# Optimization experiments

Hardware: AMD Instinct MI355X
Metric: run time of the kernel (lower is better)

Reference implementation:

```python
import jax, jax.numpy as jnp
import numpy as np
from jax import lax

K = 16  # knn_k


def _mlp(x, W1, b1, W2, b2):
    h = jax.nn.gelu(x @ W1 + b1, approximate=False)  # torch nn.GELU default = exact
    return h @ W2 + b2


def setup_inputs() -> dict:
    key = jax.random.key(0)
    ks = jax.random.split(key, 10)
    B, N, F, H = 8, 4096, 64, 128

    def xav(k, shape):
        fan_in = shape[0]
        return (jax.random.normal(k, shape, jnp.float32) / np.sqrt(fan_in)).astype(jnp.float32)

    return {
        "coords": jax.random.normal(ks[0], (B, N, 3), jnp.float32),
        "features": jax.random.normal(ks[1], (B, N, F), jnp.float32),
        "inv_W1": xav(ks[2], (6, H)), "inv_b1": jnp.zeros((H,), jnp.float32),
        "inv_W2": xav(ks[3], (H, H)), "inv_b2": jnp.zeros((H,), jnp.float32),
        "feat_W1": xav(ks[4], (F, H)), "feat_b1": jnp.zeros((H,), jnp.float32),
        "feat_W2": xav(ks[5], (H, H)), "feat_b2": jnp.zeros((H,), jnp.float32),
        "sh_W1": xav(ks[6], (2 * H, H)), "sh_b1": jnp.zeros((H,), jnp.float32),
        "sh_W2": xav(ks[7], (H, H)), "sh_b2": jnp.zeros((H,), jnp.float32),
        "g0_W": xav(ks[8], (H, 1)), "g0_b": jnp.zeros((1,), jnp.float32),
    }


def _local_geometry(coords):
    # coords: [B,N,3]
    B, N, _ = coords.shape
    k = min(K, N - 1)
    # squared pairwise distances (monotone in euclidean dist -> same kNN indices)
    sq = jnp.sum(coords * coords, axis=-1)                    # [B,N]
    dist2 = sq[:, :, None] + sq[:, None, :] - 2.0 * jnp.einsum("bnd,bmd->bnm", coords, coords)
    dist2 = lax.stop_gradient(dist2)
    eye = jnp.eye(N, dtype=bool)
    dist2 = jnp.where(eye[None], jnp.inf, dist2)
    _, idx = lax.top_k(-dist2, k)                             # smallest-k -> [B,N,k]
    neighbors = jax.vmap(lambda c, i: c[i])(coords, idx)      # [B,N,k,3]
    relative = neighbors - coords[:, :, None, :]              # [B,N,k,3]
    cov = jnp.einsum("bnki,bnkj->bnij", relative, relative) / float(k)  # [B,N,3,3]
    evals, evecs = jnp.linalg.eigh(cov)                       # ascending
    normals = evecs[..., 0]                                   # smallest-eigval eigenvector, [B,N,3]
    center = coords.mean(axis=1, keepdims=True)
    outward = coords - center
    orient = jnp.sign(jnp.sum(normals * outward, axis=-1, keepdims=True))
    orient = jnp.where(orient == 0, 1.0, orient)
    normals = normals * orient
    normals = normals / jnp.maximum(jnp.linalg.norm(normals, axis=-1, keepdims=True), 1e-6)
    radius = jnp.linalg.norm(relative, axis=-1).mean(axis=-1, keepdims=True)   # [B,N,1]
    centered_radius = jnp.linalg.norm(outward, axis=-1, keepdims=True)
    eig_sum = jnp.maximum(evals.sum(axis=-1, keepdims=True), 1e-6)
    dominance = evals[..., 2:3] / eig_sum
    invariants = jnp.concatenate([evals, radius, centered_radius, dominance], axis=-1)  # [B,N,6]
    return normals, invariants


def reference(coords, features, inv_W1, inv_b1, inv_W2, inv_b2,
              feat_W1, feat_b1, feat_W2, feat_b2,
              sh_W1, sh_b1, sh_W2, sh_b2, g0_W, g0_b):
    normals, invariants = _local_geometry(coords)
    inv_h = _mlp(invariants, inv_W1, inv_b1, inv_W2, inv_b2)
    feat_h = _mlp(features, feat_W1, feat_b1, feat_W2, feat_b2)
    hidden = _mlp(jnp.concatenate([inv_h, feat_h], axis=-1), sh_W1, sh_b1, sh_W2, sh_b2)
    scalar = hidden @ g0_W + g0_b                                   # grade 0, [B,N,1]
    plane = jnp.stack([normals[..., 0], normals[..., 1], -normals[..., 2],
                       -jnp.sum(coords * normals, axis=-1)], axis=-1)  # grade 1, [B,N,4]
    biv = jnp.concatenate([normals, jnp.zeros_like(normals)], axis=-1)  # grade 2, [B,N,6]
    point = jnp.concatenate([coords, jnp.ones(coords.shape[:-1] + (1,), coords.dtype)], axis=-1)  # grade 3 OPNS point
    zero4 = jnp.zeros(coords.shape[:-1] + (1,), coords.dtype)            # grade 4
    return jnp.concatenate([scalar, plane, biv, point, zero4], axis=-1)  # [B,N,16]
```

## Files before the change

kernel.cpp:

```cpp
#include <hip/hip_runtime.h>
#include <hip/hip_bf16.h>

#define BB 8
#define NN 4096
#define FF 64
#define HH 128
#define KNN 16

typedef __attribute__((ext_vector_type(8))) short bf16x8;
typedef __attribute__((ext_vector_type(4))) float f32x4;

#define OFF_iW2 0
#define OFF_fW1 16384
#define OFF_fW2 24576
#define OFF_sW1 40960
#define OFF_sW2 73728
#define HI_SZ   90112

__device__ __forceinline__ float sq3(float x, float y, float z) {
    return fmaf(z, z, fmaf(y, y, __fmul_rn(x, x)));
}
__device__ __forceinline__ float dist2f(float px, float py, float pz, float psq, float4 cc) {
    float t = fmaf(pz, cc.z, fmaf(py, cc.y, __fmul_rn(px, cc.x)));
    return __fsub_rn(__fadd_rn(psq, cc.w), __fmul_rn(2.0f, t));
}

__device__ __forceinline__ short f2bf(float x) {
    unsigned u = __float_as_uint(x);
    u += 0x7fffu + ((u >> 16) & 1u);
    return (short)(u >> 16);
}
__device__ __forceinline__ float bf2f(short s) {
    return __uint_as_float(((unsigned)(unsigned short)s) << 16);
}

extern "C" __global__ __launch_bounds__(256)
void k_prep(const float* __restrict__ coords, float4* __restrict__ coords4, float* __restrict__ center) {
    const int b = blockIdx.x, tid = threadIdx.x;
    __shared__ float rx[256], ry[256], rz[256];
    float sx = 0.f, sy = 0.f, sz = 0.f;
    for (int n = tid; n < NN; n += 256) {
        const float* c = coords + (size_t)(b * NN + n) * 3;
        float x = c[0], y = c[1], z = c[2];
        coords4[b * NN + n] = make_float4(x, y, z, sq3(x, y, z));
        sx += x; sy += y; sz += z;
    }
    rx[tid] = sx; ry[tid] = sy; rz[tid] = sz;
    __syncthreads();
    for (int s = 128; s > 0; s >>= 1) {
        if (tid < s) { rx[tid] += rx[tid + s]; ry[tid] += ry[tid + s]; rz[tid] += rz[tid + s]; }
        __syncthreads();
    }
    if (tid == 0) {
        center[b * 4 + 0] = rx[0] * (1.0f / NN);
        center[b * 4 + 1] = ry[0] * (1.0f / NN);
        center[b * 4 + 2] = rz[0] * (1.0f / NN);
    }
}

extern "C" __global__ __launch_bounds__(256)
void k_wprep(const float* __restrict__ iW2, const float* __restrict__ fW1,
             const float* __restrict__ fW2, const float* __restrict__ sW1,
             const float* __restrict__ sW2, short* __restrict__ wbf) {
    const int w = blockIdx.y;
    const float* W; int K; int off;
    if (w == 0)      { W = iW2; K = 128; off = OFF_iW2; }
    else if (w == 1) { W = fW1; K = 64;  off = OFF_fW1; }
    else if (w == 2) { W = fW2; K = 128; off = OFF_fW2; }
    else if (w == 3) { W = sW1; K = 256; off = OFF_sW1; }
    else             { W = sW2; K = 128; off = OFF_sW2; }
    short* hi = wbf + off;
    short* lo = wbf + HI_SZ + off;
    const int total = K * 128;
    for (int e = blockIdx.x * 256 + threadIdx.x; e < total; e += gridDim.x * 256) {
        int j = e & 7, lane = (e >> 3) & 63, ct = (e >> 9) & 7, kb = e >> 12;
        int k = kb * 32 + (lane >> 4) * 8 + j;
        int n = ct * 16 + (lane & 15);
        float v = W[k * 128 + n];
        short h = f2bf(v);
        float r = v - bf2f(h);
        hi[e] = h; lo[e] = f2bf(r);
    }
}

#define JROT(app, aqq, apq, arp, arq, vp0, vp1, vp2, vq0, vq1, vq2) { \
    float tau_ = (aqq - app) / (2.0f * apq); \
    float tt_ = copysignf(1.0f, tau_) / (fabsf(tau_) + sqrtf(1.0f + tau_ * tau_)); \
    if (apq == 0.0f) tt_ = 0.0f; \
    float cc_ = 1.0f / sqrtf(1.0f + tt_ * tt_); \
    float ss_ = tt_ * cc_; \
    float app_n = cc_*cc_*app - 2.0f*cc_*ss_*apq + ss_*ss_*aqq; \
    float aqq_n = ss_*ss_*app + 2.0f*cc_*ss_*apq + cc_*cc_*aqq; \
    float apq_n = cc_*ss_*(app - aqq) + (cc_*cc_ - ss_*ss_)*apq; \
    float arp_n = cc_*arp - ss_*arq; \
    float arq_n = ss_*arp + cc_*arq; \
    app = app_n; aqq = aqq_n; apq = apq_n; arp = arp_n; arq = arq_n; \
    float t0_ = cc_*vp0 - ss_*vq0, t1_ = cc_*vp1 - ss_*vq1, t2_ = cc_*vp2 - ss_*vq2; \
    vq0 = ss_*vp0 + cc_*vq0; vq1 = ss_*vp1 + cc_*vq1; vq2 = ss_*vp2 + cc_*vq2; \
    vp0 = t0_; vp1 = t1_; vp2 = t2_; }

#define SWAPF(a, b) { float sw_ = a; a = b; b = sw_; }

__device__ __forceinline__ void sort16(float (&d)[16]) {
#pragma unroll
    for (int k = 2; k <= 16; k <<= 1) {
#pragma unroll
        for (int j = k >> 1; j > 0; j >>= 1) {
#pragma unroll
            for (int i = 0; i < 16; i++) {
                int l = i ^ j;
                if (l > i) {
                    if ((i & k) == 0) {
                        float mn = fminf(d[i], d[l]);
                        d[l] = fmaxf(d[i], d[l]);
                        d[i] = mn;
                    } else {
                        float mx = fmaxf(d[i], d[l]);
                        d[l] = fminf(d[i], d[l]);
                        d[i] = mx;
                    }
                }
            }
        }
    }
}

__device__ __forceinline__ void merge16(float (&dk)[16], const float (&d)[16]) {
    float t[16];
#pragma unroll
    for (int i = 0; i < 16; i++) t[i] = fminf(dk[i], d[15 - i]);
#pragma unroll
    for (int j = 8; j > 0; j >>= 1) {
#pragma unroll
        for (int i = 0; i < 16; i++) {
            int l = i ^ j;
            if (l > i) {
                float mn = fminf(t[i], t[l]);
                t[l] = fmaxf(t[i], t[l]);
                t[i] = mn;
            }
        }
    }
#pragma unroll
    for (int i = 0; i < 16; i++) dk[i] = t[i];
}

__device__ __forceinline__ float gelu_exact(float x) {
    return 0.5f * x * (1.0f + erff(x * 0.70710678118654752440f));
}

template <int KDIM, int LDA>
__device__ __forceinline__ void gemm_small(const float* A, const float* __restrict__ W,
                                           const float* __restrict__ bias, int p0, int c0, float acc[4][4]) {
    float4 bb = *(const float4*)(bias + c0);
#pragma unroll
    for (int i = 0; i < 4; i++) { acc[i][0] = bb.x; acc[i][1] = bb.y; acc[i][2] = bb.z; acc[i][3] = bb.w; }
#pragma unroll
    for (int k = 0; k < KDIM; k++) {
        float4 w = *(const float4*)(W + k * HH + c0);
#pragma unroll
        for (int i = 0; i < 4; i++) {
            float a = A[(p0 + i) * LDA + k];
            acc[i][0] = fmaf(a, w.x, acc[i][0]);
            acc[i][1] = fmaf(a, w.y, acc[i][1]);
            acc[i][2] = fmaf(a, w.z, acc[i][2]);
            acc[i][3] = fmaf(a, w.w, acc[i][3]);
        }
    }
}

template <int KB, bool INIT>
__device__ __forceinline__ void gemm_mfma(const short* Ab, const short* __restrict__ whi,
                                          const short* __restrict__ wlo,
                                          const float* __restrict__ bias,
                                          int wid, int lane, f32x4 acc[2][2]) {
    const int m16 = lane & 15, quad = lane >> 4;
    if (INIT) {
        float b0 = bias[(wid * 2 + 0) * 16 + m16];
        float b1 = bias[(wid * 2 + 1) * 16 + m16];
        acc[0][0] = (f32x4){b0, b0, b0, b0}; acc[1][0] = acc[0][0];
        acc[0][1] = (f32x4){b1, b1, b1, b1}; acc[1][1] = acc[0][1];
    }
#pragma unroll 1
    for (int kb = 0; kb < KB; kb++) {
        bf16x8 a0 = *(const bf16x8*)(Ab + m16 * 136 + kb * 32 + quad * 8);
        bf16x8 a1 = *(const bf16x8*)(Ab + (m16 + 16) * 136 + kb * 32 + quad * 8);
#pragma unroll
        for (int c = 0; c < 2; c++) {
            const int off = ((kb * 8 + wid * 2 + c) * 64 + lane) * 8;
            bf16x8 bh = *(const bf16x8*)(whi + off);
            bf16x8 bl = *(const bf16x8*)(wlo + off);
            acc[0][c] = __builtin_amdgcn_mfma_f32_16x16x32_bf16(a0, bh, acc[0][c], 0, 0, 0);
            acc[0][c] = __builtin_amdgcn_mfma_f32_16x16x32_bf16(a0, bl, acc[0][c], 0, 0, 0);
            acc[1][c] = __builtin_amdgcn_mfma_f32_16x16x32_bf16(a1, bh, acc[1][c], 0, 0, 0);
            acc[1][c] = __builtin_amdgcn_mfma_f32_16x16x32_bf16(a1, bl, acc[1][c], 0, 0, 0);
        }
    }
}

__device__ __forceinline__ void acc_to_stage(float* fstage, f32x4 acc[2][2], int wid, int lane, bool dogelu) {
    const int m16 = lane & 15, quad = lane >> 4;
#pragma unroll
    for (int mt = 0; mt < 2; mt++)
#pragma unroll
        for (int c = 0; c < 2; c++)
#pragma unroll
            for (int i = 0; i < 4; i++) {
                float v = acc[mt][c][i];
                if (dogelu) v = gelu_exact(v);
                fstage[(mt * 16 + quad * 4 + i) * 128 + (wid * 2 + c) * 16 + m16] = v;
            }
}

__device__ __forceinline__ void cvt_stage(const float* fstage, short* dst, int tid) {
#pragma unroll
    for (int it = 0; it < 2; it++) {
        int idx = tid + it * 256;
        int row = idx >> 4, c8 = (idx & 15) * 8;
        const float* s = fstage + row * 128 + c8;
        float4 v0 = *(const float4*)s, v1 = *(const float4*)(s + 4);
        bf16x8 pk;
        pk[0] = f2bf(v0.x); pk[1] = f2bf(v0.y); pk[2] = f2bf(v0.z); pk[3] = f2bf(v0.w);
        pk[4] = f2bf(v1.x); pk[5] = f2bf(v1.y); pk[6] = f2bf(v1.z); pk[7] = f2bf(v1.w);
        *(bf16x8*)(dst + row * 136 + c8) = pk;
    }
}

__device__ __forceinline__ void store4f(float* dst, float a, float b, float c, float d) {
    *(float4*)dst = make_float4(a, b, c, d);
}

extern "C" __global__ __launch_bounds__(256, 4)
void k_fused(const float4* __restrict__ coords4, const float* __restrict__ center,
             const float* __restrict__ features, const short* __restrict__ wbf,
             const float* __restrict__ iW1, const float* __restrict__ ib1,
             const float* __restrict__ ib2,
             const float* __restrict__ fb1, const float* __restrict__ fb2,
             const float* __restrict__ sb1, const float* __restrict__ sb2,
             const float* __restrict__ gW, const float* __restrict__ gb,
             float* __restrict__ out) {
    const int blk = blockIdx.x;
    const int b = blk >> 7;
    const int chunk = blk & 127;
    const int tid = threadIdx.x;
    const int pid = tid & 31;
    const int h = tid >> 5;
    const int n = chunk * 32 + pid;
    const float4* __restrict__ C = coords4 + b * NN;

    __shared__ __align__(16) char smem[34944];
    float4* tile = (float4*)smem;
    int* ilist = (int*)(smem + 8192);
    int* cnts = (int*)(smem + 32768);
    float* inv8 = (float*)(smem + 33792);
    float* sc = (float*)(smem + 34816);
    float* mb = (float*)ilist;
    float* fstage = (float*)smem;
    short* Abf = (short*)(smem + 16384);
    short* FHbf = (short*)(smem + 25088);

    float4 me = C[n];
    const float px = me.x, py = me.y, pz = me.z, psq = me.w;
    const float INF = __builtin_inff();

    float dk[KNN];
#pragma unroll
    for (int i = 0; i < KNN; i++) dk[i] = INF;

    for (int r = 0; r < 8; r++) {
        __syncthreads();
#pragma unroll
        for (int e = tid; e < 512; e += 256) {
            int seg = e >> 6, idx = e & 63;
            tile[e] = C[seg * 512 + r * 64 + idx];
        }
        __syncthreads();
        const float4* T = &tile[h * 64];
        const int selfj = n - (h * 512 + r * 64);
#pragma unroll
        for (int bt = 0; bt < 4; bt++) {
            float d[16];
#pragma unroll
            for (int i = 0; i < 16; i++) {
                float4 cc = T[bt * 16 + i];
                float dd = dist2f(px, py, pz, psq, cc);
                d[i] = (bt * 16 + i) == selfj ? INF : dd;
            }
            sort16(d);
            merge16(dk, d);
        }
    }

    __syncthreads();
#pragma unroll
    for (int i = 0; i < KNN; i++) mb[tid * 17 + i] = dk[i];
    __syncthreads();
#pragma unroll
    for (int p = 1; p < 8; p++) {
        const int partner = (((h + p) & 7) << 5) + pid;
        float o[16];
#pragma unroll
        for (int i = 0; i < KNN; i++) o[i] = mb[partner * 17 + i];
        merge16(dk, o);
    }
    const float d15 = dk[15];

    int cs = 0, ct = 0;
    const int lbase = (pid * 8 + h) * 24;
    for (int r = 0; r < 8; r++) {
        __syncthreads();
#pragma unroll
        for (int e = tid; e < 512; e += 256) {
            int seg = e >> 6, idx = e & 63;
            tile[e] = C[seg * 512 + r * 64 + idx];
        }
        __syncthreads();
        const float4* T = &tile[h * 64];
        const int base = h * 512 + r * 64;
#pragma unroll 4
        for (int j = 0; j < 64; j++) {
            float4 cc = T[j];
            float d = dist2f(px, py, pz, psq, cc);
            int g = base + j;
            if (g != n && d <= d15) {
                if (d < d15) {
                    if (cs < 15) ilist[lbase + cs] = g;
                    cs++;
                } else if (ct < 8) {
                    ilist[lbase + 15 + ct] = g;
                    ct++;
                }
            }
        }
    }
    cnts[pid * 8 + h] = (cs & 0xff) | (ct << 8);
    __syncthreads();

    if (h == 0) {
        int s[8], t8[8], sb[8], tb[8], cum[8], tcum[8];
#pragma unroll
        for (int q = 0; q < 8; q++) {
            int cp = cnts[pid * 8 + q];
            s[q] = cp & 0xff; t8[q] = cp >> 8;
            sb[q] = (pid * 8 + q) * 24; tb[q] = sb[q] + 15;
        }
        cum[0] = s[0]; tcum[0] = t8[0];
#pragma unroll
        for (int q = 1; q < 8; q++) { cum[q] = cum[q - 1] + s[q]; tcum[q] = tcum[q - 1] + t8[q]; }

        float cxx = 0.f, cxy = 0.f, cxz = 0.f, cyy = 0.f, cyz = 0.f, czz = 0.f, radsum = 0.f;
#pragma unroll
        for (int j = 0; j < KNN; j++) {
            int addr = sb[0] + j;
#pragma unroll
            for (int q = 1; q < 8; q++)
                if (j >= cum[q - 1]) addr = sb[q] + (j - cum[q - 1]);
            int jt = j - cum[7];
            if (j >= cum[7]) addr = tb[0] + jt;
#pragma unroll
            for (int q = 1; q < 8; q++)
                if (j >= cum[7] && jt >= tcum[q - 1]) addr = tb[q] + (jt - tcum[q - 1]);
            int id = ilist[addr];
            float4 cc = C[id];
            float rx = __fsub_rn(cc.x, px), ry = __fsub_rn(cc.y, py), rz = __fsub_rn(cc.z, pz);
            cxx = __fadd_rn(cxx, __fmul_rn(rx, rx));
            cxy = __fadd_rn(cxy, __fmul_rn(rx, ry));
            cxz = __fadd_rn(cxz, __fmul_rn(rx, rz));
            cyy = __fadd_rn(cyy, __fmul_rn(ry, ry));
            cyz = __fadd_rn(cyz, __fmul_rn(ry, rz));
            czz = __fadd_rn(czz, __fmul_rn(rz, rz));
            float rr = __fadd_rn(__fadd_rn(__fmul_rn(rx, rx), __fmul_rn(ry, ry)), __fmul_rn(rz, rz));
            radsum = __fadd_rn(radsum, sqrtf(rr));
        }
        const float inv_k = 1.0f / KNN;
        float a00 = cxx * inv_k, a01 = cxy * inv_k, a02 = cxz * inv_k;
        float a11 = cyy * inv_k, a12 = cyz * inv_k, a22 = czz * inv_k;

        float V00 = 1.f, V01 = 0.f, V02 = 0.f;
        float V10 = 0.f, V11 = 1.f, V12 = 0.f;
        float V20 = 0.f, V21 = 0.f, V22 = 1.f;
        for (int sweep = 0; sweep < 6; sweep++) {
            JROT(a00, a11, a01, a02, a12, V00, V10, V20, V01, V11, V21);
            JROT(a00, a22, a02, a01, a12, V00, V10, V20, V02, V12, V22);
            JROT(a11, a22, a12, a01, a02, V01, V11, V21, V02, V12, V22);
        }
        float e0 = a00, e1 = a11, e2 = a22;
        float x0 = V00, y0 = V10, z0 = V20;
        float x1 = V01, y1 = V11, z1 = V21;
        float x2 = V02, y2 = V12, z2 = V22;
        if (e0 > e1) { SWAPF(e0, e1); SWAPF(x0, x1); SWAPF(y0, y1); SWAPF(z0, z1); }
        if (e1 > e2) { SWAPF(e1, e2); SWAPF(x1, x2); SWAPF(y1, y2); SWAPF(z1, z2); }
        if (e0 > e1) { SWAPF(e0, e1); SWAPF(x0, x1); SWAPF(y0, y1); SWAPF(z0, z1); }

        float cx = center[b * 4 + 0], cy = center[b * 4 + 1], cz = center[b * 4 + 2];
        float ox = __fsub_rn(px, cx), oy = __fsub_rn(py, cy), oz = __fsub_rn(pz, cz);
        float dt = __fadd_rn(__fadd_rn(__fmul_rn(x0, ox), __fmul_rn(y0, oy)), __fmul_rn(z0, oz));
        float sgn = (dt >= 0.0f) ? 1.0f : -1.0f;
        x0 *= sgn; y0 *= sgn; z0 *= sgn;
        float nrm = sqrtf(__fadd_rn(__fadd_rn(__fmul_rn(x0, x0), __fmul_rn(y0, y0)), __fmul_rn(z0, z0)));
        float den = fmaxf(nrm, 1e-6f);
        x0 = x0 / den; y0 = y0 / den; z0 = z0 / den;

        float radius = radsum * inv_k;
        float crad = sqrtf(__fadd_rn(__fadd_rn(__fmul_rn(ox, ox), __fmul_rn(oy, oy)), __fmul_rn(oz, oz)));
        float esum = fmaxf(__fadd_rn(__fadd_rn(e0, e1), e2), 1e-6f);
        float dom = e2 / esum;

        float* ip = inv8 + pid * 8;
        ip[0] = e0; ip[1] = e1; ip[2] = e2; ip[3] = radius; ip[4] = crad; ip[5] = dom;
        ip[6] = 0.f; ip[7] = 0.f;

        float pd = __fadd_rn(__fadd_rn(__fmul_rn(px, x0), __fmul_rn(py, y0)), __fmul_rn(pz, z0));
        float4* o = (float4*)(out + (size_t)(b * NN + n) * 16);
        o[0] = make_float4(0.0f, x0, y0, -z0);
        o[1] = make_float4(-pd, x0, y0, z0);
        o[2] = make_float4(0.0f, 0.0f, 0.0f, px);
        o[3] = make_float4(py, pz, 1.0f, 0.0f);
        sc[pid] = gb[0];
    }
    __syncthreads();

    const int wid = tid >> 6, lane = tid & 63;
    const short* w_iW2h = wbf + OFF_iW2; const short* w_iW2l = wbf + HI_SZ + OFF_iW2;
    const short* w_fW1h = wbf + OFF_fW1; const short* w_fW1l = wbf + HI_SZ + OFF_fW1;
    const short* w_fW2h = wbf + OFF_fW2; const short* w_fW2l = wbf + HI_SZ + OFF_fW2;
    const short* w_sW1h = wbf + OFF_sW1; const short* w_sW1l = wbf + HI_SZ + OFF_sW1;
    const short* w_sW2h = wbf + OFF_sW2; const short* w_sW2l = wbf + HI_SZ + OFF_sW2;
    f32x4 acc[2][2];

    {
        int row = tid >> 3, c8 = (tid & 7) * 8;
        const float* s = features + (size_t)(b * NN + chunk * 32 + row) * FF + c8;
        float4 v0 = *(const float4*)s, v1 = *(const float4*)(s + 4);
        bf16x8 pk;
        pk[0] = f2bf(v0.x); pk[1] = f2bf(v0.y); pk[2] = f2bf(v0.z); pk[3] = f2bf(v0.w);
        pk[4] = f2bf(v1.x); pk[5] = f2bf(v1.y); pk[6] = f2bf(v1.z); pk[7] = f2bf(v1.w);
        *(bf16x8*)(Abf + row * 136 + c8) = pk;
    }
    __syncthreads();

    gemm_mfma<2, true>(Abf, w_fW1h, w_fW1l, fb1, wid, lane, acc);
    acc_to_stage(fstage, acc, wid, lane, true);
    __syncthreads();
    cvt_stage(fstage, Abf, tid);
    __syncthreads();

    gemm_mfma<4, true>(Abf, w_fW2h, w_fW2l, fb2, wid, lane, acc);
    acc_to_stage(fstage, acc, wid, lane, false);
    __syncthreads();
    cvt_stage(fstage, FHbf, tid);
    __syncthreads();

    {
        const int cg = tid & 31, pg = tid >> 5;
        const int c0 = cg * 4, p0 = pg * 4;
        float a4[4][4];
        gemm_small<6, 8>(inv8, iW1, ib1, p0, c0, a4);
#pragma unroll
        for (int i = 0; i < 4; i++)
            store4f(&fstage[(p0 + i) * 128 + c0], gelu_exact(a4[i][0]), gelu_exact(a4[i][1]),
                    gelu_exact(a4[i][2]), gelu_exact(a4[i][3]));
    }
    __syncthreads();
    cvt_stage(fstage, Abf, tid);
    __syncthreads();

    gemm_mfma<4, true>(Abf, w_iW2h, w_iW2l, ib2, wid, lane, acc);
    acc_to_stage(fstage, acc, wid, lane, false);
    __syncthreads();
    cvt_stage(fstage, Abf, tid);
    __syncthreads();

    gemm_mfma<4, true>(Abf, w_sW1h, w_sW1l, sb1, wid, lane, acc);
    gemm_mfma<4, false>(FHbf, w_sW1h + 16384, w_sW1l + 16384, nullptr, wid, lane, acc);
    acc_to_stage(fstage, acc, wid, lane, true);
    __syncthreads();
    cvt_stage(fstage, Abf, tid);
    __syncthreads();

    gemm_mfma<4, true>(Abf, w_sW2h, w_sW2l, sb2, wid, lane, acc);
    {
        const int m16 = lane & 15, quad = lane >> 4;
#pragma unroll
        for (int mt = 0; mt < 2; mt++)
#pragma unroll
            for (int c = 0; c < 2; c++) {
                float g = gW[(wid * 2 + c) * 16 + m16];
#pragma unroll
                for (int i = 0; i < 4; i++)
                    atomicAdd(&sc[mt * 16 + quad * 4 + i], acc[mt][c][i] * g);
            }
    }
    __syncthreads();
    if (tid < 32) out[(size_t)(b * NN + n) * 16] = sc[tid];
}

extern "C" void kernel_launch(void* const* d_in, const int* in_sizes, int n_in,
                              void* d_out, int out_size, void* d_ws, size_t ws_size,
                              hipStream_t stream) {
    const float* coords   = (const float*)d_in[0];
    const float* features = (const float*)d_in[1];
    const float* iW1 = (const float*)d_in[2],  * ib1 = (const float*)d_in[3];
    const float* iW2 = (const float*)d_in[4],  * ib2 = (const float*)d_in[5];
    const float* fW1 = (const float*)d_in[6],  * fb1 = (const float*)d_in[7];
    const float* fW2 = (const float*)d_in[8],  * fb2 = (const float*)d_in[9];
    const float* sW1 = (const float*)d_in[10], * sb1 = (const float*)d_in[11];
    const float* sW2 = (const float*)d_in[12], * sb2 = (const float*)d_in[13];
    const float* gW  = (const float*)d_in[14], * gb  = (const float*)d_in[15];
    float* out = (float*)d_out;

    float* ws = (float*)d_ws;
    float4* coords4 = (float4*)ws;
    float* center = ws + BB * NN * 4;
    short* wbf = (short*)((char*)d_ws + 524416);

    hipLaunchKernelGGL(k_prep, dim3(BB), dim3(256), 0, stream, coords, coords4, center);
    hipLaunchKernelGGL(k_wprep, dim3(16, 5), dim3(256), 0, stream, iW2, fW1, fW2, sW1, sW2, wbf);
    hipLaunchKernelGGL(k_fused, dim3(1024), dim3(256), 0, stream, coords4, center, features, wbf,
                       iW1, ib1, ib2, fb1, fb2, sb1, sb2, gW, gb, out);
}
```

Before: 286.7 us.

## Shrink LDS footprint by writing bf16 directly and packing neighbor indices

Removes the fp32 staging buffer between MLP layers: accumulators are converted to bf16 and written straight into the A operand buffer, with a barrier before each write so the buffer can be reused in place. Neighbor candidate indices are stored as 16-bit shorts with a 23-slot stride, and the merge buffer aliases the tile region. Together these cut shared memory from about 35KB to 22KB, and launch bounds are raised to 7 blocks per CU to exploit the extra occupancy. The tradeoffs are possible register spills under the tighter register budget and scalar bf16 stores that may cause LDS bank conflicts.

```diff
diff --git a/kernel.cpp b/kernel.cpp
--- a/kernel.cpp
+++ b/kernel.cpp
@@ -198,7 +198,7 @@
     }
 }
 
-__device__ __forceinline__ void acc_to_stage(float* fstage, f32x4 acc[2][2], int wid, int lane, bool dogelu) {
+__device__ __forceinline__ void acc_to_bf(short* dst, f32x4 acc[2][2], int wid, int lane, bool dogelu) {
     const int m16 = lane & 15, quad = lane >> 4;
 #pragma unroll
     for (int mt = 0; mt < 2; mt++)
@@ -208,29 +208,11 @@
             for (int i = 0; i < 4; i++) {
                 float v = acc[mt][c][i];
                 if (dogelu) v = gelu_exact(v);
-                fstage[(mt * 16 + quad * 4 + i) * 128 + (wid * 2 + c) * 16 + m16] = v;
-            }
-}
-
-__device__ __forceinline__ void cvt_stage(const float* fstage, short* dst, int tid) {
-#pragma unroll
-    for (int it = 0; it < 2; it++) {
-        int idx = tid + it * 256;
-        int row = idx >> 4, c8 = (idx & 15) * 8;
-        const float* s = fstage + row * 128 + c8;
-        float4 v0 = *(const float4*)s, v1 = *(const float4*)(s + 4);
-        bf16x8 pk;
-        pk[0] = f2bf(v0.x); pk[1] = f2bf(v0.y); pk[2] = f2bf(v0.z); pk[3] = f2bf(v0.w);
-        pk[4] = f2bf(v1.x); pk[5] = f2bf(v1.y); pk[6] = f2bf(v1.z); pk[7] = f2bf(v1.w);
-        *(bf16x8*)(dst + row * 136 + c8) = pk;
-    }
-}
-
-__device__ __forceinline__ void store4f(float* dst, float a, float b, float c, float d) {
-    *(float4*)dst = make_float4(a, b, c, d);
-}
-
-extern "C" __global__ __launch_bounds__(256, 4)
+                dst[(mt * 16 + quad * 4 + i) * 136 + (wid * 2 + c) * 16 + m16] = f2bf(v);
+            }
+}
+
+extern "C" __global__ __launch_bounds__(256, 7)
 void k_fused(const float4* __restrict__ coords4, const float* __restrict__ center,
              const float* __restrict__ features, const short* __restrict__ wbf,
              const float* __restrict__ iW1, const float* __restrict__ ib1,
@@ -248,16 +230,15 @@
     const int n = chunk * 32 + pid;
     const float4* __restrict__ C = coords4 + b * NN;
 
-    __shared__ __align__(16) char smem[34944];
+    __shared__ __align__(16) char smem[22144];
     float4* tile = (float4*)smem;
-    int* ilist = (int*)(smem + 8192);
-    int* cnts = (int*)(smem + 32768);
-    float* inv8 = (float*)(smem + 33792);
-    float* sc = (float*)(smem + 34816);
-    float* mb = (float*)ilist;
-    float* fstage = (float*)smem;
-    short* Abf = (short*)(smem + 16384);
-    short* FHbf = (short*)(smem + 25088);
+    short* ilist = (short*)(smem + 8192);
+    int* cnts = (int*)(smem + 19968);
+    float* inv8 = (float*)(smem + 20992);
+    float* sc = (float*)(smem + 22016);
+    float* mb = (float*)smem;
+    short* Abf = (short*)smem;
+    short* FHbf = (short*)(smem + 8704);
 
     float4 me = C[n];
     const float px = me.x, py = me.y, pz = me.z, psq = me.w;
@@ -306,7 +287,7 @@
     const float d15 = dk[15];
 
     int cs = 0, ct = 0;
-    const int lbase = (pid * 8 + h) * 24;
+    const int lbase = (pid * 8 + h) * 23;
     for (int r = 0; r < 8; r++) {
         __syncthreads();
 #pragma unroll
@@ -324,10 +305,10 @@
             int g = base + j;
             if (g != n && d <= d15) {
                 if (d < d15) {
-                    if (cs < 15) ilist[lbase + cs] = g;
+                    if (cs < 15) ilist[lbase + cs] = (short)g;
                     cs++;
                 } else if (ct < 8) {
-                    ilist[lbase + 15 + ct] = g;
+                    ilist[lbase + 15 + ct] = (short)g;
                     ct++;
                 }
             }
@@ -342,7 +323,7 @@
         for (int q = 0; q < 8; q++) {
             int cp = cnts[pid * 8 + q];
             s[q] = cp & 0xff; t8[q] = cp >> 8;
-            sb[q] = (pid * 8 + q) * 24; tb[q] = sb[q] + 15;
+            sb[q] = (pid * 8 + q) * 23; tb[q] = sb[q] + 15;
         }
         cum[0] = s[0]; tcum[0] = t8[0];
 #pragma unroll
@@ -440,15 +421,13 @@
     __syncthreads();
 
     gemm_mfma<2, true>(Abf, w_fW1h, w_fW1l, fb1, wid, lane, acc);
-    acc_to_stage(fstage, acc, wid, lane, true);
-    __syncthreads();
-    cvt_stage(fstage, Abf, tid);
+    __syncthreads();
+    acc_to_bf(Abf, acc, wid, lane, true);
     __syncthreads();
 
     gemm_mfma<4, true>(Abf, w_fW2h, w_fW2l, fb2, wid, lane, acc);
-    acc_to_stage(fstage, acc, wid, lane, false);
-    __syncthreads();
-    cvt_stage(fstage, FHbf, tid);
+    __syncthreads();
+    acc_to_bf(FHbf, acc, wid, lane, false);
     __syncthreads();
 
     {
@@ -458,24 +437,21 @@
         gemm_small<6, 8>(inv8, iW1, ib1, p0, c0, a4);
 #pragma unroll
         for (int i = 0; i < 4; i++)
-            store4f(&fstage[(p0 + i) * 128 + c0], gelu_exact(a4[i][0]), gelu_exact(a4[i][1]),
-                    gelu_exact(a4[i][2]), gelu_exact(a4[i][3]));
-    }
-    __syncthreads();
-    cvt_stage(fstage, Abf, tid);
+#pragma unroll
+            for (int j = 0; j < 4; j++)
+                Abf[(p0 + i) * 136 + c0 + j] = f2bf(gelu_exact(a4[i][j]));
+    }
     __syncthreads();
 
     gemm_mfma<4, true>(Abf, w_iW2h, w_iW2l, ib2, wid, lane, acc);
-    acc_to_stage(fstage, acc, wid, lane, false);
-    __syncthreads();
-    cvt_stage(fstage, Abf, tid);
+    __syncthreads();
+    acc_to_bf(Abf, acc, wid, lane, false);
     __syncthreads();
 
     gemm_mfma<4, true>(Abf, w_sW1h, w_sW1l, sb1, wid, lane, acc);
     gemm_mfma<4, false>(FHbf, w_sW1h + 16384, w_sW1l + 16384, nullptr, wid, lane, acc);
-    acc_to_stage(fstage, acc, wid, lane, true);
-    __syncthreads();
-    cvt_stage(fstage, Abf, tid);
+    __syncthreads();
+    acc_to_bf(Abf, acc, wid, lane, true);
     __syncthreads();
 
     gemm_mfma<4, true>(Abf, w_sW2h, w_sW2l, sb2, wid, lane, acc);
```

Result: no change. 290.1 us (+1.2%).
